# Performance work log

Measured on AMD Instinct MI355X. Metric: run time of the kernel, lower is better.

## Reference

```python
import jax, jax.numpy as jnp
import numpy as np

B, T, C, H = 4, 2048, 1024, 16
D = C // H  # head_size = 64


def setup_inputs() -> dict:
    key = jax.random.key(0)
    k1, k2, k3 = jax.random.split(key, 3)
    s = 1.0 / np.sqrt(C)
    return {
        "x": jax.random.normal(k1, (B, T, C), dtype=jnp.float32),
        "w_qkv": jax.random.normal(k2, (3 * C, C), dtype=jnp.float32) * s,
        "w_out": jax.random.normal(k3, (C, C), dtype=jnp.float32) * s,
        "b_out": jnp.zeros((C,), dtype=jnp.float32),
    }


def reference(x, w_qkv, w_out, b_out):
    Bx, Tx, Cx = x.shape
    qkv = x @ w_qkv.T                                # [B,T,3C]
    q, k, v = jnp.split(qkv, 3, axis=2)
    # [B,T,C] -> [B,H,T,D]
    q = q.reshape(Bx, Tx, H, D).transpose(0, 2, 1, 3)
    k = k.reshape(Bx, Tx, H, D).transpose(0, 2, 1, 3)
    v = v.reshape(Bx, Tx, H, D).transpose(0, 2, 1, 3)
    scores = jnp.einsum('bhqd,bhkd->bhqk', q, k) / jnp.sqrt(jnp.float32(D))
    causal = jnp.tril(jnp.ones((Tx, Tx), dtype=bool))
    scores = jnp.where(causal[None, None], scores, -jnp.inf)
    attn = jax.nn.softmax(scores, axis=-1)
    out = jnp.einsum('bhqk,bhkd->bhqd', attn, v)     # [B,H,T,D]
    out = out.transpose(0, 2, 1, 3).reshape(Bx, Tx, Cx)
    return out @ w_out.T + b_out
```

## Files before the change

### kernel.cpp

```cpp
#include <hip/hip_runtime.h>

constexpr int Bn = 4, Tn = 2048, Cn = 1024, Hn = 16, Dn = 64;

typedef __attribute__((ext_vector_type(8))) short short8;
typedef __attribute__((ext_vector_type(4))) float floatx4;
typedef __attribute__((ext_vector_type(2))) unsigned uint2v;

#define DEVFN __device__ __forceinline__

constexpr float SCL = 0.18033688011112042f;

DEVFN unsigned f2bf_u(float f) {
  unsigned u = __builtin_bit_cast(unsigned, f);
  u += 0x7fffu + ((u >> 16) & 1u);
  return u >> 16;
}
DEVFN short f2bf(float f) { return (short)f2bf_u(f); }

DEVFN floatx4 mfma16(short8 a, short8 b, floatx4 c) {
  return __builtin_amdgcn_mfma_f32_16x16x32_bf16(a, b, c, 0, 0, 0);
}

DEVFN void gld_lds16(const void* g, void* l) {
  __builtin_amdgcn_global_load_lds(
      (const __attribute__((address_space(1))) unsigned*)g,
      (__attribute__((address_space(3))) unsigned*)l, 16, 0, 0);
}

constexpr int G_X = 8192 * 1024 / 8;
constexpr int G_WQ = 3072 * 1024 / 8;
constexpr int G_WO = 1024 * 1024 / 8;
__global__ __launch_bounds__(256) void cast3_kernel(
    const float* __restrict__ x, const float* __restrict__ wq,
    const float* __restrict__ wo, short* __restrict__ dst) {
  const int i = blockIdx.x * 256 + threadIdx.x;
  const float* src;
  int rel;
  if (i < G_X) {
    src = x; rel = i;
  } else if (i < G_X + G_WQ) {
    src = wq; rel = i - G_X;
  } else {
    src = wo; rel = i - (G_X + G_WQ);
  }
  const floatx4* p = (const floatx4*)src + (size_t)rel * 2;
  floatx4 a = p[0], b = p[1];
  short8 r;
  r[0] = f2bf(a[0]); r[1] = f2bf(a[1]); r[2] = f2bf(a[2]); r[3] = f2bf(a[3]);
  r[4] = f2bf(b[0]); r[5] = f2bf(b[1]); r[6] = f2bf(b[2]); r[7] = f2bf(b[3]);
  ((short8*)dst)[i] = r;
}

template <int MODE>
__global__ __launch_bounds__(256, 2) void gemm_bt(
    const short* __restrict__ A, const short* __restrict__ Bw, int M, int N, int K,
    short* __restrict__ qkb, short* __restrict__ vtb,
    const float* __restrict__ bias, float* __restrict__ fout) {
  __shared__ short As[128 * 64];
  __shared__ short Bs[128 * 64];
  const int tid = threadIdx.x;
  const int lane = tid & 63, wave = tid >> 6;
  const int l15 = lane & 15, quad = lane >> 4;
  const int wr = wave >> 1, wc = wave & 1;
  const int m0 = blockIdx.x * 128, n0 = blockIdx.y * 128;

  const int r0 = tid >> 3, cs = tid & 7;
  const short* Ag = A + (size_t)(m0 + r0) * K + (cs ^ (r0 & 7)) * 8;
  const short* Bg = Bw + (size_t)(n0 + r0) * K + (cs ^ (r0 & 7)) * 8;

  floatx4 acc[4][4] = {};

  for (int k0 = 0; k0 < K; k0 += 64) {
#pragma unroll
    for (int it = 0; it < 4; ++it) {
      gld_lds16(Ag + k0 + (size_t)(it * 32) * K, As + it * 2048 + tid * 8);
      gld_lds16(Bg + k0 + (size_t)(it * 32) * K, Bs + it * 2048 + tid * 8);
    }
    __syncthreads();
#pragma unroll
    for (int ks = 0; ks < 2; ++ks) {
      short8 af[4], bf[4];
#pragma unroll
      for (int i = 0; i < 4; ++i) {
        const int row = wr * 64 + i * 16 + l15;
        af[i] = *(const short8*)(As + row * 64 +
                                 ((ks * 4 + quad) ^ (l15 & 7)) * 8);
      }
#pragma unroll
      for (int i = 0; i < 4; ++i) {
        const int row = wc * 64 + i * 16 + l15;
        bf[i] = *(const short8*)(Bs + row * 64 +
                                 ((ks * 4 + quad) ^ (l15 & 7)) * 8);
      }
#pragma unroll
      for (int mi = 0; mi < 4; ++mi)
#pragma unroll
        for (int ni = 0; ni < 4; ++ni)
          acc[mi][ni] = mfma16(af[mi], bf[ni], acc[mi][ni]);
    }
    __syncthreads();
  }

#pragma unroll
  for (int mi = 0; mi < 4; ++mi) {
    const int row0 = m0 + wr * 64 + mi * 16 + quad * 4;
#pragma unroll
    for (int ni = 0; ni < 4; ++ni) {
      const int col = n0 + wc * 64 + ni * 16 + l15;
      if constexpr (MODE == 0) {
        if (col < 2 * Cn) {
#pragma unroll
          for (int r = 0; r < 4; ++r) {
            float v = acc[mi][ni][r];
            if (col < Cn) v *= SCL;
            qkb[(size_t)(row0 + r) * (2 * Cn) + col] = f2bf(v);
          }
        } else {
          const int hc = col - 2 * Cn;
          const int hh = hc >> 6, d = hc & 63;
          const int bb = row0 >> 11, t = row0 & (Tn - 1);
          uint2v pk;
          pk[0] = f2bf_u(acc[mi][ni][0]) | (f2bf_u(acc[mi][ni][1]) << 16);
          pk[1] = f2bf_u(acc[mi][ni][2]) | (f2bf_u(acc[mi][ni][3]) << 16);
          *(uint2v*)(vtb + ((size_t)((bb * Hn + hh) * Dn + d)) * Tn + t) = pk;
        }
      } else {
#pragma unroll
        for (int r = 0; r < 4; ++r)
          fout[(size_t)(row0 + r) * N + col] = acc[mi][ni][r] + bias[col];
      }
    }
  }
}

__global__ __launch_bounds__(256, 3) void attn_kernel(
    const short* __restrict__ qk, const short* __restrict__ vt,
    short* __restrict__ att) {
  __shared__ short Ks[2][64 * 64];
  __shared__ short Vs[2][64 * 64];
  __shared__ short Ps[4][16 * 64];

  const int bh = blockIdx.x;
  const int qt = 15 - blockIdx.y;
  const int b = bh >> 4, h = bh & 15;
  const int tid = threadIdx.x;
  const int lane = tid & 63, wave = tid >> 6;
  const int l15 = lane & 15, quad = lane >> 4;
  const int q0w = qt * 128 + wave * 32;

  const short* qbase = qk + (size_t)(b * Tn) * 2048 + h * 64;
  const short* kbase = qbase + 1024;
  const short* vbase = vt + (size_t)(bh * 64) * Tn;
  short* pw = Ps[wave];

  short8 qf[2][2];
#pragma unroll
  for (int f = 0; f < 2; ++f)
#pragma unroll
    for (int ks = 0; ks < 2; ++ks)
      qf[f][ks] = *(const short8*)(qbase + (size_t)(q0w + f * 16 + l15) * 2048 +
                                   ks * 32 + quad * 8);

  floatx4 o[2][4] = {};
  float lpart[2] = {0.f, 0.f};

  const int wave_nt = ((q0w + 31) >> 6) + 1;
  const int block_nt = 2 * qt + 2;

  const int jr = tid >> 3;
  const int cl = tid & 7;

#define STAGE(JT, BUF)                                                       \
  {                                                                          \
    const int j0s = (JT) * 64;                                               \
    _Pragma("unroll") for (int it = 0; it < 2; ++it) {                       \
      const int row = jr + it * 32;                                          \
      const int cg = cl ^ (row & 7);                                         \
      gld_lds16(kbase + (size_t)(j0s + row) * 2048 + cg * 8,                 \
                &Ks[BUF][it * 2048 + tid * 8]);                              \
      gld_lds16(vbase + (size_t)row * Tn + j0s + cg * 8,                     \
                &Vs[BUF][it * 2048 + tid * 8]);                              \
    }                                                                        \
  }

  STAGE(0, 0)
  __syncthreads();

  for (int jt = 0; jt < block_nt; ++jt) {
    const int buf = jt & 1;
    if (jt + 1 < block_nt) STAGE(jt + 1, buf ^ 1)

    if (jt < wave_nt) {
      const int j0 = jt * 64;

      floatx4 st[2][4];
#pragma unroll
      for (int f = 0; f < 2; ++f)
#pragma unroll
        for (int nj = 0; nj < 4; ++nj) st[f][nj] = floatx4{0.f, 0.f, 0.f, 0.f};
#pragma unroll
      for (int half = 0; half < 2; ++half) {
        short8 kfa[2][2];
#pragma unroll
        for (int j2 = 0; j2 < 2; ++j2)
#pragma unroll
          for (int ks = 0; ks < 2; ++ks) {
            const int cld = (ks * 4 + quad) ^ (l15 & 7);
            kfa[j2][ks] = *(const short8*)(
                &Ks[buf][((half * 2 + j2) * 16 + l15) * 64 + cld * 8]);
          }
#pragma unroll
        for (int f = 0; f < 2; ++f)
#pragma unroll
          for (int j2 = 0; j2 < 2; ++j2)
#pragma unroll
            for (int ks = 0; ks < 2; ++ks)
              st[f][half * 2 + j2] =
                  mfma16(kfa[j2][ks], qf[f][ks], st[f][half * 2 + j2]);
      }

      short8 vf[4][2];
#pragma unroll
      for (int nd = 0; nd < 4; ++nd)
#pragma unroll
        for (int ks = 0; ks < 2; ++ks) {
          const int cld = (ks * 4 + quad) ^ (l15 & 7);
          vf[nd][ks] =
              *(const short8*)(&Vs[buf][(nd * 16 + l15) * 64 + cld * 8]);
        }

#pragma unroll
      for (int f = 0; f < 2; ++f) {
        const bool need_mask = (j0 + 63 > q0w + f * 16);
        const int ig = q0w + f * 16 + l15;
#pragma unroll
        for (int nj = 0; nj < 4; ++nj) {
          float p[4];
#pragma unroll
          for (int r = 0; r < 4; ++r) {
            float e = __builtin_amdgcn_exp2f(st[f][nj][r]);
            if (need_mask) {
              const int jg = j0 + nj * 16 + quad * 4 + r;
              e = (jg > ig) ? 0.f : e;
            }
            lpart[f] += e;
            p[r] = e;
          }
          const int c = nj * 2 + (quad >> 1);
          const int cld = c ^ (l15 & 7);
          uint2v pk;
          pk[0] = f2bf_u(p[0]) | (f2bf_u(p[1]) << 16);
          pk[1] = f2bf_u(p[2]) | (f2bf_u(p[3]) << 16);
          *(uint2v*)(&pw[l15 * 64 + cld * 8 + (quad & 1) * 4]) = pk;
        }
        __asm__ volatile("s_waitcnt lgkmcnt(0)" ::: "memory");

        short8 pf[2];
#pragma unroll
        for (int ks = 0; ks < 2; ++ks) {
          const int cld = (ks * 4 + quad) ^ (l15 & 7);
          pf[ks] = *(const short8*)(&pw[l15 * 64 + cld * 8]);
        }
#pragma unroll
        for (int nd = 0; nd < 4; ++nd)
#pragma unroll
          for (int ks = 0; ks < 2; ++ks)
            o[f][nd] = mfma16(vf[nd][ks], pf[ks], o[f][nd]);
        __asm__ volatile("" ::: "memory");
      }
    }
    __syncthreads();
  }

  float inv[2];
#pragma unroll
  for (int f = 0; f < 2; ++f) {
    float s2 = lpart[f];
    s2 += __shfl_xor(s2, 16);
    s2 += __shfl_xor(s2, 32);
    inv[f] = 1.0f / s2;
  }

#pragma unroll
  for (int f = 0; f < 2; ++f) {
#pragma unroll
    for (int nd = 0; nd < 4; ++nd) {
      const int c = nd * 2 + (quad >> 1);
      const int cld = c ^ (l15 & 7);
      uint2v pk;
      pk[0] =
          f2bf_u(o[f][nd][0] * inv[f]) | (f2bf_u(o[f][nd][1] * inv[f]) << 16);
      pk[1] =
          f2bf_u(o[f][nd][2] * inv[f]) | (f2bf_u(o[f][nd][3] * inv[f]) << 16);
      *(uint2v*)(&pw[l15 * 64 + cld * 8 + (quad & 1) * 4]) = pk;
    }
    __asm__ volatile("s_waitcnt lgkmcnt(0)" ::: "memory");
#pragma unroll
    for (int ps = 0; ps < 2; ++ps) {
      const int r16 = ps * 8 + (lane >> 3);
      const int cn = lane & 7;
      const int cldr = cn ^ (r16 & 7);
      const short8 val = *(const short8*)(&pw[r16 * 64 + cldr * 8]);
      *(short8*)(att + (size_t)(b * Tn + q0w + f * 16 + r16) * Cn + h * 64 +
                 cn * 8) = val;
    }
    __asm__ volatile("" ::: "memory");
  }
#undef STAGE
}

extern "C" void kernel_launch(void* const* d_in, const int* in_sizes, int n_in,
                              void* d_out, int out_size, void* d_ws,
                              size_t ws_size, hipStream_t stream) {
  const float* x = (const float*)d_in[0];
  const float* w_qkv = (const float*)d_in[1];
  const float* w_out = (const float*)d_in[2];
  const float* b_out = (const float*)d_in[3];
  float* out = (float*)d_out;

  short* xb = (short*)d_ws;
  short* wqb = xb + (size_t)8192 * 1024;
  short* wob = wqb + (size_t)3072 * 1024;
  short* qkb = wob + (size_t)1024 * 1024;
  short* vtb = qkb + (size_t)8192 * 2048;
  short* att = xb;

  cast3_kernel<<<dim3((G_X + G_WQ + G_WO) / 256), 256, 0, stream>>>(
      x, w_qkv, w_out, xb);

  gemm_bt<0><<<dim3(64, 24), 256, 0, stream>>>(xb, wqb, 8192, 3072, 1024, qkb,
                                               vtb, nullptr, nullptr);
  attn_kernel<<<dim3(64, 16), 256, 0, stream>>>(qkb, vtb, att);
  gemm_bt<1><<<dim3(64, 8), 256, 0, stream>>>(att, wob, 8192, 1024, 1024,
                                              nullptr, nullptr, b_out, out);
}
```

Measured before the change: 238.6 us.

## Add 256x256 double-buffered ping-pong QKV GEMM kernel with XCD-aware tile remap

Replaces the generic 128x128 QKV projection GEMM with a dedicated 512-thread kernel using 256x256 output tiles, double-buffered LDS loaded via global_load_lds, and an interleaved schedule of LDS reads, async global stages and MFMA blocks separated by barriers with raised wave priority. Block indices are remapped so consecutive tiles land on the same XCD for L2 reuse. The intent is higher data reuse per tile and overlap of memory with matrix math. The cost is large LDS use (128KB) and register pressure, and fewer blocks (384) than before, which may leave CUs underused.

```diff
diff --git a/kernel.cpp b/kernel.cpp
--- a/kernel.cpp
+++ b/kernel.cpp
@@ -49,6 +49,140 @@
   r[0] = f2bf(a[0]); r[1] = f2bf(a[1]); r[2] = f2bf(a[2]); r[3] = f2bf(a[3]);
   r[4] = f2bf(b[0]); r[5] = f2bf(b[1]); r[6] = f2bf(b[2]); r[7] = f2bf(b[3]);
   ((short8*)dst)[i] = r;
+}
+
+#define FENCE() __asm__ volatile("" ::: "memory")
+#define BAR8() { FENCE(); __builtin_amdgcn_s_barrier(); FENCE(); }
+#define VMW(n) __asm__ volatile("s_waitcnt vmcnt(" #n ")" ::: "memory")
+
+__global__ __launch_bounds__(512, 2) void gemm_qkv(
+    const short* __restrict__ A, const short* __restrict__ Bw,
+    short* __restrict__ qkb, short* __restrict__ vtb) {
+  __shared__ __align__(16) short As[2][256 * 64];
+  __shared__ __align__(16) short Bs[2][256 * 64];
+
+  const int tid = threadIdx.x;
+  const int lane = tid & 63;
+  const int wave = tid >> 6;
+  const int l15 = lane & 15, quad = lane >> 4;
+  const int wr = wave >> 2, wc = wave & 3;
+
+  const int orig = blockIdx.y * 32 + blockIdx.x;
+  const int wg = (orig & 7) * 48 + (orig >> 3);
+  const int m0 = (wg & 31) * 256, n0 = (wg >> 5) * 256;
+
+  const int r0 = tid >> 3, cs = tid & 7;
+  const short* Ag = A + (size_t)(m0 + r0) * 1024 + (cs ^ (r0 & 7)) * 8;
+  const short* Bg = Bw + (size_t)(n0 + r0) * 1024 + (cs ^ (r0 & 7)) * 8;
+  short* Asl = (short*)As + tid * 8;
+  short* Bsl = (short*)Bs + tid * 8;
+
+#define STG(ls, gp, buf_, tile_, h_)                                    \
+  {                                                                     \
+    gld_lds16(gp + (tile_) * 64 + (size_t)((h_) * 128) * 1024,          \
+              ls + (buf_) * 16384 + (h_) * 8192);                       \
+    gld_lds16(gp + (tile_) * 64 + (size_t)((h_) * 128 + 64) * 1024,     \
+              ls + (buf_) * 16384 + (h_) * 8192 + 4096);                \
+  }
+
+  short8 af[4][2];
+  short8 bf[2][2][2];
+  floatx4 acc[8][4] = {};
+
+#define RDA(mh_, buf_)                                                        \
+  _Pragma("unroll") for (int mi = 0; mi < 4; ++mi)                            \
+  _Pragma("unroll") for (int ks = 0; ks < 2; ++ks)                            \
+      af[mi][ks] = *(const short8*)(                                          \
+          (const short*)As + (buf_) * 16384 +                                 \
+          (((mh_) * 4 + mi) * 32 + wr * 16 + l15) * 64 +                      \
+          ((ks * 4 + quad) ^ (l15 & 7)) * 8);
+
+#define RDB(nh_, buf_)                                                        \
+  _Pragma("unroll") for (int ni = 0; ni < 2; ++ni)                            \
+  _Pragma("unroll") for (int ks = 0; ks < 2; ++ks)                            \
+      bf[nh_][ni][ks] = *(const short8*)(                                     \
+          (const short*)Bs + (buf_) * 16384 +                                 \
+          (((nh_) * 2 + ni) * 64 + wc * 16 + l15) * 64 +                      \
+          ((ks * 4 + quad) ^ (l15 & 7)) * 8);
+
+#define MMA(mh_, nh_)                                                         \
+  __builtin_amdgcn_s_setprio(1);                                              \
+  _Pragma("unroll") for (int mi = 0; mi < 4; ++mi)                            \
+  _Pragma("unroll") for (int ni = 0; ni < 2; ++ni)                            \
+  _Pragma("unroll") for (int ks = 0; ks < 2; ++ks)                            \
+      acc[(mh_) * 4 + mi][(nh_) * 2 + ni] = mfma16(                           \
+          af[mi][ks], bf[nh_][ni][ks], acc[(mh_) * 4 + mi][(nh_) * 2 + ni]);  \
+  __builtin_amdgcn_s_setprio(0);
+
+  STG(Asl, Ag, 0, 0, 0) STG(Asl, Ag, 0, 0, 1)
+  STG(Bsl, Bg, 0, 0, 0) STG(Bsl, Bg, 0, 0, 1)
+  STG(Asl, Ag, 1, 1, 0) STG(Bsl, Bg, 1, 1, 0) STG(Bsl, Bg, 1, 1, 1)
+  VMW(6);
+  BAR8();
+
+#pragma unroll 1
+  for (int tp = 0; tp < 7; ++tp) {
+    const int t2 = 2 * tp + 2, t3 = 2 * tp + 3;
+    RDA(0, 0) RDB(0, 0) STG(Asl, Ag, 1, 2 * tp + 1, 1)
+    BAR8(); MMA(0, 0) BAR8();
+    RDB(1, 0) STG(Asl, Ag, 0, t2, 0)
+    BAR8(); MMA(0, 1) BAR8();
+    RDA(1, 0) STG(Bsl, Bg, 0, t2, 0)
+    BAR8(); MMA(1, 0) BAR8();
+    STG(Bsl, Bg, 0, t2, 1)
+    BAR8(); MMA(1, 1) VMW(6); BAR8();
+    RDA(0, 1) RDB(0, 1) STG(Asl, Ag, 0, t2, 1)
+    BAR8(); MMA(0, 0) BAR8();
+    RDB(1, 1) STG(Asl, Ag, 1, t3, 0)
+    BAR8(); MMA(0, 1) BAR8();
+    RDA(1, 1) STG(Bsl, Bg, 1, t3, 0)
+    BAR8(); MMA(1, 0) BAR8();
+    STG(Bsl, Bg, 1, t3, 1)
+    BAR8(); MMA(1, 1) VMW(6); BAR8();
+  }
+  RDA(0, 0) RDB(0, 0) STG(Asl, Ag, 1, 15, 1)
+  BAR8(); MMA(0, 0) BAR8();
+  RDB(1, 0)
+  BAR8(); MMA(0, 1) BAR8();
+  RDA(1, 0)
+  BAR8(); MMA(1, 0) BAR8();
+  MMA(1, 1) VMW(0); BAR8();
+  RDA(0, 1) RDB(0, 1)
+  BAR8(); MMA(0, 0) BAR8();
+  RDB(1, 1)
+  BAR8(); MMA(0, 1) BAR8();
+  RDA(1, 1)
+  BAR8(); MMA(1, 0) BAR8();
+  MMA(1, 1)
+
+#pragma unroll
+  for (int mi = 0; mi < 8; ++mi) {
+    const int row0 = m0 + mi * 32 + wr * 16 + quad * 4;
+#pragma unroll
+    for (int ni = 0; ni < 4; ++ni) {
+      const int col = n0 + ni * 64 + wc * 16 + l15;
+      if (col < 2 * Cn) {
+#pragma unroll
+        for (int r = 0; r < 4; ++r) {
+          float v = acc[mi][ni][r];
+          if (col < Cn) v *= SCL;
+          qkb[(size_t)(row0 + r) * (2 * Cn) + col] = f2bf(v);
+        }
+      } else {
+        const int hc = col - 2 * Cn;
+        const int hh = hc >> 6, d = hc & 63;
+        const int bb = row0 >> 11, t = row0 & (Tn - 1);
+        uint2v pk;
+        pk[0] = f2bf_u(acc[mi][ni][0]) | (f2bf_u(acc[mi][ni][1]) << 16);
+        pk[1] = f2bf_u(acc[mi][ni][2]) | (f2bf_u(acc[mi][ni][3]) << 16);
+        *(uint2v*)(vtb + ((size_t)((bb * Hn + hh) * Dn + d)) * Tn + t) = pk;
+      }
+    }
+  }
+#undef STG
+#undef RDA
+#undef RDB
+#undef MMA
 }
 
 template <int MODE>
@@ -328,8 +462,7 @@
   cast3_kernel<<<dim3((G_X + G_WQ + G_WO) / 256), 256, 0, stream>>>(
       x, w_qkv, w_out, xb);
 
-  gemm_bt<0><<<dim3(64, 24), 256, 0, stream>>>(xb, wqb, 8192, 3072, 1024, qkb,
-                                               vtb, nullptr, nullptr);
+  gemm_qkv<<<dim3(32, 12), 512, 0, stream>>>(xb, wqb, qkb, vtb);
   attn_kernel<<<dim3(64, 16), 256, 0, stream>>>(qkb, vtb, att);
   gemm_bt<1><<<dim3(64, 8), 256, 0, stream>>>(att, wob, 8192, 1024, 1024,
                                               nullptr, nullptr, b_out, out);
```

Result: slower. 254.8 us (+6.8%).
